# Kernel optimization log

Hardware: AMD Instinct MI355X
Metric: run time of the kernel (lower is better)

## Reference

```python
import jax, jax.numpy as jnp
import numpy as np

SCALING = 2.0
EPS = 1e-8


def setup_inputs() -> dict:
    key = jax.random.key(0)
    k_x, k_a, k_b = jax.random.split(key, 3)
    N, B, S, H, R = 8, 2, 2048, 4096, 64
    x = jax.random.normal(k_x, (B, S, H), dtype=jnp.float32)
    lora_A = jax.random.normal(k_a, (N, H, R), dtype=jnp.float32)
    # torch init is zeros for B, but use small random values so the norm-rescale path is exercised
    lora_B = jax.random.normal(k_b, (N, R, H), dtype=jnp.float32) * 0.02
    return {"x": x, "lora_A": lora_A, "lora_B": lora_B}


def reference(x, lora_A, lora_B):
    # x: [B,S,H]; lora_A: [N,H,R]; lora_B: [N,R,H]
    intermediate = jnp.einsum('bsh,nhr->nbsr', x, lora_A)          # [N,B,S,R]
    updates = jnp.einsum('nbsr,nrh->nbsh', intermediate, lora_B)   # [N,B,S,H]
    norms = jnp.linalg.norm(updates, axis=-1, keepdims=True) + EPS
    updates = updates / norms * SCALING
    return x[None] + updates                                       # [N,B,S,H]
```

## Files before the change

### kernel.cpp

```cpp
#include <hip/hip_runtime.h>
#include <hip/hip_bf16.h>

#define NL 8
#define HD 4096
#define RD 64
#define MD 4096
#define NGC 512

typedef __bf16 bf16x8 __attribute__((ext_vector_type(8)));
typedef float f32x4 __attribute__((ext_vector_type(4)));
typedef unsigned short ushort8 __attribute__((ext_vector_type(8)));
typedef float float4v __attribute__((ext_vector_type(4)));

__device__ __forceinline__ unsigned short f2bf(float f) {
    union { __hip_bfloat16 b; unsigned short u; } c;
    c.b = __float2bfloat16(f);
    return c.u;
}

__device__ __forceinline__ void gload_lds16(const void* g, void* l) {
    auto gp = (const __attribute__((address_space(1))) unsigned int*)(g);
    auto lp = (__attribute__((address_space(3))) unsigned int*)(l);
    __builtin_amdgcn_global_load_lds(gp, lp, 16, 0, 0);
}

__global__ __launch_bounds__(256) void k_prep(const float* __restrict__ A,
                                              const float* __restrict__ B,
                                              unsigned short* __restrict__ At,
                                              unsigned short* __restrict__ Bt) {
    __shared__ unsigned short T[64][65];
    int t = threadIdx.x;
    int bb = blockIdx.x;
    if (bb < 512) {
        int n = bb >> 6;
        int h0 = (bb & 63) << 6;
        const float* src = A + (size_t)n * HD * RD;
#pragma unroll
        for (int rep = 0; rep < 16; ++rep) {
            int flat = rep * 256 + t;
            int hh = flat >> 6, rr = flat & 63;
            T[hh][rr] = f2bf(src[(size_t)(h0 + hh) * RD + rr]);
        }
        __syncthreads();
#pragma unroll
        for (int rep = 0; rep < 16; ++rep) {
            int flat = rep * 256 + t;
            int rr = flat >> 6, hh = flat & 63;
            At[(size_t)(n * RD + rr) * HD + h0 + hh] = T[hh][rr];
        }
    } else {
        int b2 = bb - 512;
        int n = b2 >> 6;
        int h0 = (b2 & 63) << 6;
        const float* src = B + (size_t)n * RD * HD;
#pragma unroll
        for (int rep = 0; rep < 16; ++rep) {
            int flat = rep * 256 + t;
            int rr = flat >> 6, hh = flat & 63;
            T[rr][hh] = f2bf(src[(size_t)rr * HD + h0 + hh]);
        }
        __syncthreads();
        unsigned short* dst = Bt + (size_t)n * HD * RD;
#pragma unroll
        for (int rep = 0; rep < 16; ++rep) {
            int flat = rep * 256 + t;
            int hh = flat >> 6, rr = flat & 63;
            dst[(size_t)(h0 + hh) * RD + rr] = T[rr][hh];
        }
    }
}

__global__ __launch_bounds__(256) void k_gram(const float* __restrict__ B,
                                              float* __restrict__ Gp) {
    __shared__ float Bl[64][129];
    int t = threadIdx.x;
    int n = blockIdx.x >> 5;
    int c = blockIdx.x & 31;
    int k0 = c << 7;
    const float* src = B + (size_t)n * RD * HD + k0;
#pragma unroll
    for (int rep = 0; rep < 8; ++rep) {
        int flat = (rep * 256 + t) * 4;
        int rr = flat >> 7, hh = flat & 127;
        float4v v = *(const float4v*)(src + (size_t)rr * HD + hh);
        Bl[rr][hh] = v[0]; Bl[rr][hh + 1] = v[1];
        Bl[rr][hh + 2] = v[2]; Bl[rr][hh + 3] = v[3];
    }
    __syncthreads();
    int i0 = (t >> 4) << 2;
    int j0 = (t & 15) << 2;
    float acc[4][4];
#pragma unroll
    for (int a = 0; a < 4; ++a)
#pragma unroll
        for (int b = 0; b < 4; ++b) acc[a][b] = 0.f;
    for (int h = 0; h < 128; ++h) {
        float bi[4], bj[4];
#pragma unroll
        for (int a = 0; a < 4; ++a) { bi[a] = Bl[i0 + a][h]; bj[a] = Bl[j0 + a][h]; }
#pragma unroll
        for (int a = 0; a < 4; ++a)
#pragma unroll
            for (int b = 0; b < 4; ++b) acc[a][b] += bi[a] * bj[b];
    }
    float* g = Gp + (size_t)(n * 32 + c) * RD * RD;
#pragma unroll
    for (int a = 0; a < 4; ++a)
#pragma unroll
        for (int b = 0; b < 4; ++b)
            g[(i0 + a) * RD + j0 + b] = acc[a][b];
}

__global__ __launch_bounds__(256) void k_gram_reduce(const float* __restrict__ Gp,
                                                     float* __restrict__ G) {
    int idx = blockIdx.x * 256 + threadIdx.x;
    int n = idx >> 12;
    int rem = idx & 4095;
    const float* src = Gp + (size_t)n * 32 * 4096 + rem;
    float sum = 0.f;
#pragma unroll
    for (int c = 0; c < 32; ++c) sum += src[(size_t)c * 4096];
    G[idx] = sum;
}

__global__ __launch_bounds__(256) void k_gemm1(const float* __restrict__ x,
                                               const unsigned short* __restrict__ At,
                                               float* __restrict__ inter_p) {
    __shared__ unsigned short As[2][64 * 64];
    __shared__ unsigned short Bs[2][128 * 64];
    int t = threadIdx.x, lane = t & 63;
    int bid = blockIdx.x;
    int ks = bid & 1;
    int c0 = ((bid >> 1) & 3) * 128;
    int m0 = (bid >> 3) * 64;
    int kbase = ks * 2048;

    int sa_r0 = t >> 3, sa_sg = t & 7;
    int sa_sw = sa_sg ^ (sa_r0 & 7);
    const float* xrow0 = x + (size_t)(m0 + sa_r0) * HD + sa_sg * 8;
    const float* xrow1 = x + (size_t)(m0 + sa_r0 + 32) * HD + sa_sg * 8;

    int wv = t >> 6;
    int wm = (wv >> 1) * 32;
    int wc = (wv & 1) * 64;

    f32x4 acc[4][2];
#pragma unroll
    for (int cf = 0; cf < 4; ++cf)
#pragma unroll
        for (int mf = 0; mf < 2; ++mf) acc[cf][mf] = (f32x4){0.f, 0.f, 0.f, 0.f};

    {
#pragma unroll
        for (int q = 0; q < 4; ++q) {
            int flat = q * 256 + t;
            int cc = flat >> 3, sg = flat & 7;
            int sw = sg ^ (cc & 7);
            gload_lds16(At + (size_t)(c0 + cc) * HD + kbase + sw * 8,
                        (void*)&Bs[0][(q * 256 + (t & ~63)) * 8]);
        }
        float4v a0 = *(const float4v*)(xrow0 + kbase);
        float4v a1 = *(const float4v*)(xrow0 + kbase + 4);
        float4v b0 = *(const float4v*)(xrow1 + kbase);
        float4v b1 = *(const float4v*)(xrow1 + kbase + 4);
        ushort8 sva, svb;
#pragma unroll
        for (int j = 0; j < 4; ++j) {
            sva[j] = f2bf(a0[j]); sva[j + 4] = f2bf(a1[j]);
            svb[j] = f2bf(b0[j]); svb[j + 4] = f2bf(b1[j]);
        }
        *(ushort8*)&As[0][sa_r0 * 64 + sa_sw * 8] = sva;
        *(ushort8*)&As[0][(sa_r0 + 32) * 64 + sa_sw * 8] = svb;
    }
    __syncthreads();

    float4v pa0, pa1, pb0, pb1;
    for (int kt = 0; kt < 32; ++kt) {
        int cur = kt & 1;
        int knext = kbase + (kt + 1) * 64;
        if (kt < 31) {
#pragma unroll
            for (int q = 0; q < 4; ++q) {
                int flat = q * 256 + t;
                int cc = flat >> 3, sg = flat & 7;
                int sw = sg ^ (cc & 7);
                gload_lds16(At + (size_t)(c0 + cc) * HD + knext + sw * 8,
                            (void*)&Bs[cur ^ 1][(q * 256 + (t & ~63)) * 8]);
            }
            pa0 = *(const float4v*)(xrow0 + knext);
            pa1 = *(const float4v*)(xrow0 + knext + 4);
            pb0 = *(const float4v*)(xrow1 + knext);
            pb1 = *(const float4v*)(xrow1 + knext + 4);
        }
        const unsigned short* as = As[cur];
        const unsigned short* bs = Bs[cur];
#pragma unroll
        for (int kk = 0; kk < 2; ++kk) {
            int seg = kk * 4 + (lane >> 4);
            bf16x8 a_c[4], b_x[2];
#pragma unroll
            for (int cf = 0; cf < 4; ++cf) {
                int row = wc + cf * 16 + (lane & 15);
                a_c[cf] = *(const bf16x8*)&bs[row * 64 + (seg ^ (row & 7)) * 8];
            }
#pragma unroll
            for (int mf = 0; mf < 2; ++mf) {
                int col = wm + mf * 16 + (lane & 15);
                b_x[mf] = *(const bf16x8*)&as[col * 64 + (seg ^ (col & 7)) * 8];
            }
#pragma unroll
            for (int cf = 0; cf < 4; ++cf)
#pragma unroll
                for (int mf = 0; mf < 2; ++mf)
                    acc[cf][mf] = __builtin_amdgcn_mfma_f32_16x16x32_bf16(
                        a_c[cf], b_x[mf], acc[cf][mf], 0, 0, 0);
        }
        if (kt < 31) {
            ushort8 sva, svb;
#pragma unroll
            for (int j = 0; j < 4; ++j) {
                sva[j] = f2bf(pa0[j]); sva[j + 4] = f2bf(pa1[j]);
                svb[j] = f2bf(pb0[j]); svb[j + 4] = f2bf(pb1[j]);
            }
            *(ushort8*)&As[cur ^ 1][sa_r0 * 64 + sa_sw * 8] = sva;
            *(ushort8*)&As[cur ^ 1][(sa_r0 + 32) * 64 + sa_sw * 8] = svb;
        }
        __syncthreads();
    }
    float* dst = inter_p + (size_t)ks * MD * NGC;
#pragma unroll
    for (int mf = 0; mf < 2; ++mf) {
        int m = m0 + wm + mf * 16 + (lane & 15);
#pragma unroll
        for (int cf = 0; cf < 4; ++cf) {
            int c = c0 + wc + cf * 16 + (lane >> 4) * 4;
            *(float4v*)&dst[(size_t)m * NGC + c] = acc[cf][mf];
        }
    }
}

__global__ __launch_bounds__(256) void k_scale(const float* __restrict__ inter_p,
                                               const float* __restrict__ G,
                                               float* __restrict__ s,
                                               unsigned short* __restrict__ interbf) {
    __shared__ float Gs[64][65];
    __shared__ float Ib[4][8][64];
    int t = threadIdx.x, lane = t & 63, wv = t >> 6;
    int n = blockIdx.x >> 7;
    int m0 = (blockIdx.x & 127) << 5;
    const float* gsrc = G + n * 4096;
#pragma unroll
    for (int rep = 0; rep < 16; ++rep) {
        int flat = rep * 256 + t;
        Gs[flat >> 6][flat & 63] = gsrc[flat];
    }
#pragma unroll
    for (int r = 0; r < 8; ++r) {
        int m = m0 + wv * 8 + r;
        size_t off = (size_t)m * NGC + n * RD + lane;
        float Iv = inter_p[off] + inter_p[(size_t)MD * NGC + off];
        interbf[off] = f2bf(Iv);
        Ib[wv][r][lane] = Iv;
    }
    __syncthreads();
    float greg[64];
#pragma unroll
    for (int j = 0; j < 64; ++j) greg[j] = Gs[lane][j];
#pragma unroll
    for (int r = 0; r < 8; ++r) {
        const float* ib = Ib[wv][r];
        float t0 = 0.f, t1 = 0.f, t2 = 0.f, t3 = 0.f;
#pragma unroll
        for (int j = 0; j < 64; j += 4) {
            t0 += greg[j]     * ib[j];
            t1 += greg[j + 1] * ib[j + 1];
            t2 += greg[j + 2] * ib[j + 2];
            t3 += greg[j + 3] * ib[j + 3];
        }
        float pl = ((t0 + t1) + (t2 + t3)) * ib[lane];
#pragma unroll
        for (int o = 32; o; o >>= 1) pl += __shfl_xor(pl, o);
        if (lane == 0) {
            int m = m0 + wv * 8 + r;
            s[n * MD + m] = 2.0f / (sqrtf(fmaxf(pl, 0.f)) + 1e-8f);
        }
    }
}

__global__ __launch_bounds__(256, 2) void k_gemm2(const float* __restrict__ x,
                                                  const unsigned short* __restrict__ interbf,
                                                  const unsigned short* __restrict__ Bt,
                                                  const float* __restrict__ s,
                                                  float* __restrict__ out) {
    __shared__ unsigned short As[2][64 * 64];
    __shared__ unsigned short Bs[2][256 * 64];
    int t = threadIdx.x, lane = t & 63, wv = t >> 6;
    int b = blockIdx.x;
    int xcd = b & 7;
    int idx = b >> 3;
    int h0 = (xcd * 2 + (idx >> 6)) * 256;
    int m0 = (idx & 63) * 64;

    int wm = (wv >> 1) * 32;
    int wh = (wv & 1) * 128;

#pragma unroll
    for (int q = 0; q < 8; ++q) {
        int flat = q * 256 + t;
        int h = flat >> 3, sg = flat & 7;
        int sw = sg ^ (h & 7);
        gload_lds16(Bt + (size_t)(0 * HD + h0 + h) * RD + sw * 8,
                    (void*)&Bs[0][(q * 256 + (t & ~63)) * 8]);
    }
#pragma unroll
    for (int q = 0; q < 2; ++q) {
        int flat = q * 256 + t;
        int m = flat >> 3, sg = flat & 7;
        int sw = sg ^ (m & 7);
        gload_lds16(interbf + (size_t)(m0 + m) * NGC + 0 * RD + sw * 8,
                    (void*)&As[0][(q * 256 + (t & ~63)) * 8]);
    }
    float4v xv[2][8];
#pragma unroll
    for (int mf = 0; mf < 2; ++mf) {
        int m = m0 + wm + mf * 16 + (lane & 15);
#pragma unroll
        for (int hf = 0; hf < 8; ++hf) {
            int h = h0 + wh + hf * 16 + (lane >> 4) * 4;
            xv[mf][hf] = *(const float4v*)&x[(size_t)m * HD + h];
        }
    }
    asm volatile("s_waitcnt vmcnt(0)" ::: "memory");
    __syncthreads();

    for (int n = 0; n < NL; ++n) {
        int cur = n & 1;
        if (n < NL - 1) {
#pragma unroll
            for (int q = 0; q < 8; ++q) {
                int flat = q * 256 + t;
                int h = flat >> 3, sg = flat & 7;
                int sw = sg ^ (h & 7);
                gload_lds16(Bt + (size_t)((n + 1) * HD + h0 + h) * RD + sw * 8,
                            (void*)&Bs[cur ^ 1][(q * 256 + (t & ~63)) * 8]);
            }
#pragma unroll
            for (int q = 0; q < 2; ++q) {
                int flat = q * 256 + t;
                int m = flat >> 3, sg = flat & 7;
                int sw = sg ^ (m & 7);
                gload_lds16(interbf + (size_t)(m0 + m) * NGC + (n + 1) * RD + sw * 8,
                            (void*)&As[cur ^ 1][(q * 256 + (t & ~63)) * 8]);
            }
        }
        asm volatile("" ::: "memory");

        f32x4 acc[8][2];
#pragma unroll
        for (int hf = 0; hf < 8; ++hf)
#pragma unroll
            for (int mf = 0; mf < 2; ++mf) acc[hf][mf] = (f32x4){0.f, 0.f, 0.f, 0.f};

        const unsigned short* as = As[cur];
        const unsigned short* bs = Bs[cur];
#pragma unroll
        for (int kk = 0; kk < 2; ++kk) {
            int seg = kk * 4 + (lane >> 4);
            bf16x8 a_h[8], b_m[2];
#pragma unroll
            for (int hf = 0; hf < 8; ++hf) {
                int row = wh + hf * 16 + (lane & 15);
                a_h[hf] = *(const bf16x8*)&bs[row * 64 + (seg ^ (row & 7)) * 8];
            }
#pragma unroll
            for (int mf = 0; mf < 2; ++mf) {
                int col = wm + mf * 16 + (lane & 15);
                b_m[mf] = *(const bf16x8*)&as[col * 64 + (seg ^ (col & 7)) * 8];
            }
#pragma unroll
            for (int hf = 0; hf < 8; ++hf)
#pragma unroll
                for (int mf = 0; mf < 2; ++mf)
                    acc[hf][mf] = __builtin_amdgcn_mfma_f32_16x16x32_bf16(
                        a_h[hf], b_m[mf], acc[hf][mf], 0, 0, 0);
        }

        size_t obase = (size_t)n * MD * HD;
#pragma unroll
        for (int mf = 0; mf < 2; ++mf) {
            int m = m0 + wm + mf * 16 + (lane & 15);
            float sv = s[n * MD + m];
#pragma unroll
            for (int hf = 0; hf < 8; ++hf) {
                int h = h0 + wh + hf * 16 + (lane >> 4) * 4;
                float4v r;
#pragma unroll
                for (int j = 0; j < 4; ++j) r[j] = xv[mf][hf][j] + sv * acc[hf][mf][j];
                *(float4v*)&out[obase + (size_t)m * HD + h] = r;
            }
        }
        if (n < NL - 1) {
            asm volatile("s_waitcnt vmcnt(16)\n\ts_barrier" ::: "memory");
        }
    }
}

extern "C" void kernel_launch(void* const* d_in, const int* in_sizes, int n_in,
                              void* d_out, int out_size, void* d_ws, size_t ws_size,
                              hipStream_t stream) {
    const float* x = (const float*)d_in[0];
    const float* lA = (const float*)d_in[1];
    const float* lB = (const float*)d_in[2];
    float* out = (float*)d_out;
    char* ws = (char*)d_ws;
    unsigned short* At      = (unsigned short*)(ws);
    unsigned short* Bt      = (unsigned short*)(ws + 4194304);
    float*          inter_p = (float*)(ws + 8388608);
    float*          Gp      = (float*)(ws + 25165824);
    float*          G       = (float*)(ws + 29360128);
    float*          s       = (float*)(ws + 29491200);
    unsigned short* interbf = (unsigned short*)(ws + 29622272);

    k_prep<<<1024, 256, 0, stream>>>(lA, lB, At, Bt);
    k_gram<<<256, 256, 0, stream>>>(lB, Gp);
    k_gram_reduce<<<128, 256, 0, stream>>>(Gp, G);
    k_gemm1<<<512, 256, 0, stream>>>(x, At, inter_p);
    k_scale<<<1024, 256, 0, stream>>>(inter_p, G, s, interbf);
    k_gemm2<<<1024, 256, 0, stream>>>(x, interbf, Bt, s, out);
}
```

Baseline: 218.2 us.

## Merge prep/gram launches and widen gemm1 M-tile to 128 rows

Folds the weight transpose/convert and the partial Gram computation into one kernel, and runs the Gram reduction as extra blocks inside gemm1, cutting two kernel launches. gemm1's M tile doubles from 64 to 128 rows, with four 16-row fragments per wave, so each At tile loaded from global memory is reused across more rows. The price is more LDS and accumulator registers per block and half as many gemm1 blocks (256 instead of 512), which may leave the GPU under-occupied.

```diff
diff --git a/kernel.cpp b/kernel.cpp
--- a/kernel.cpp
+++ b/kernel.cpp
@@ -24,11 +24,13 @@
     __builtin_amdgcn_global_load_lds(gp, lp, 16, 0, 0);
 }
 
-__global__ __launch_bounds__(256) void k_prep(const float* __restrict__ A,
-                                              const float* __restrict__ B,
-                                              unsigned short* __restrict__ At,
-                                              unsigned short* __restrict__ Bt) {
-    __shared__ unsigned short T[64][65];
+__global__ __launch_bounds__(256) void k_setup(const float* __restrict__ A,
+                                               const float* __restrict__ B,
+                                               unsigned short* __restrict__ At,
+                                               unsigned short* __restrict__ Bt,
+                                               float* __restrict__ Gp) {
+    __shared__ float BUF[64 * 129];
+    unsigned short* T = (unsigned short*)BUF;
     int t = threadIdx.x;
     int bb = blockIdx.x;
     if (bb < 512) {
@@ -39,16 +41,16 @@
         for (int rep = 0; rep < 16; ++rep) {
             int flat = rep * 256 + t;
             int hh = flat >> 6, rr = flat & 63;
-            T[hh][rr] = f2bf(src[(size_t)(h0 + hh) * RD + rr]);
+            T[hh * 65 + rr] = f2bf(src[(size_t)(h0 + hh) * RD + rr]);
         }
         __syncthreads();
 #pragma unroll
         for (int rep = 0; rep < 16; ++rep) {
             int flat = rep * 256 + t;
             int rr = flat >> 6, hh = flat & 63;
-            At[(size_t)(n * RD + rr) * HD + h0 + hh] = T[hh][rr];
-        }
-    } else {
+            At[(size_t)(n * RD + rr) * HD + h0 + hh] = T[hh * 65 + rr];
+        }
+    } else if (bb < 1024) {
         int b2 = bb - 512;
         int n = b2 >> 6;
         int h0 = (b2 & 63) << 6;
@@ -57,7 +59,7 @@
         for (int rep = 0; rep < 16; ++rep) {
             int flat = rep * 256 + t;
             int rr = flat >> 6, hh = flat & 63;
-            T[rr][hh] = f2bf(src[(size_t)rr * HD + h0 + hh]);
+            T[rr * 65 + hh] = f2bf(src[(size_t)rr * HD + h0 + hh]);
         }
         __syncthreads();
         unsigned short* dst = Bt + (size_t)n * HD * RD;
@@ -65,90 +67,90 @@
         for (int rep = 0; rep < 16; ++rep) {
             int flat = rep * 256 + t;
             int hh = flat >> 6, rr = flat & 63;
-            dst[(size_t)(h0 + hh) * RD + rr] = T[rr][hh];
-        }
-    }
-}
-
-__global__ __launch_bounds__(256) void k_gram(const float* __restrict__ B,
-                                              float* __restrict__ Gp) {
-    __shared__ float Bl[64][129];
-    int t = threadIdx.x;
-    int n = blockIdx.x >> 5;
-    int c = blockIdx.x & 31;
-    int k0 = c << 7;
-    const float* src = B + (size_t)n * RD * HD + k0;
-#pragma unroll
-    for (int rep = 0; rep < 8; ++rep) {
-        int flat = (rep * 256 + t) * 4;
-        int rr = flat >> 7, hh = flat & 127;
-        float4v v = *(const float4v*)(src + (size_t)rr * HD + hh);
-        Bl[rr][hh] = v[0]; Bl[rr][hh + 1] = v[1];
-        Bl[rr][hh + 2] = v[2]; Bl[rr][hh + 3] = v[3];
-    }
-    __syncthreads();
-    int i0 = (t >> 4) << 2;
-    int j0 = (t & 15) << 2;
-    float acc[4][4];
-#pragma unroll
-    for (int a = 0; a < 4; ++a)
-#pragma unroll
-        for (int b = 0; b < 4; ++b) acc[a][b] = 0.f;
-    for (int h = 0; h < 128; ++h) {
-        float bi[4], bj[4];
-#pragma unroll
-        for (int a = 0; a < 4; ++a) { bi[a] = Bl[i0 + a][h]; bj[a] = Bl[j0 + a][h]; }
+            dst[(size_t)(h0 + hh) * RD + rr] = T[rr * 65 + hh];
+        }
+    } else {
+        int g = bb - 1024;
+        int n = g >> 5;
+        int c = g & 31;
+        int k0 = c << 7;
+        float* Bl = BUF;
+        const float* src = B + (size_t)n * RD * HD + k0;
+#pragma unroll
+        for (int rep = 0; rep < 8; ++rep) {
+            int flat = (rep * 256 + t) * 4;
+            int rr = flat >> 7, hh = flat & 127;
+            float4v v = *(const float4v*)(src + (size_t)rr * HD + hh);
+            Bl[rr * 129 + hh] = v[0]; Bl[rr * 129 + hh + 1] = v[1];
+            Bl[rr * 129 + hh + 2] = v[2]; Bl[rr * 129 + hh + 3] = v[3];
+        }
+        __syncthreads();
+        int i0 = (t >> 4) << 2;
+        int j0 = (t & 15) << 2;
+        float acc[4][4];
 #pragma unroll
         for (int a = 0; a < 4; ++a)
 #pragma unroll
-            for (int b = 0; b < 4; ++b) acc[a][b] += bi[a] * bj[b];
-    }
-    float* g = Gp + (size_t)(n * 32 + c) * RD * RD;
-#pragma unroll
-    for (int a = 0; a < 4; ++a)
-#pragma unroll
-        for (int b = 0; b < 4; ++b)
-            g[(i0 + a) * RD + j0 + b] = acc[a][b];
-}
-
-__global__ __launch_bounds__(256) void k_gram_reduce(const float* __restrict__ Gp,
-                                                     float* __restrict__ G) {
-    int idx = blockIdx.x * 256 + threadIdx.x;
-    int n = idx >> 12;
-    int rem = idx & 4095;
-    const float* src = Gp + (size_t)n * 32 * 4096 + rem;
-    float sum = 0.f;
-#pragma unroll
-    for (int c = 0; c < 32; ++c) sum += src[(size_t)c * 4096];
-    G[idx] = sum;
+            for (int b = 0; b < 4; ++b) acc[a][b] = 0.f;
+        for (int h = 0; h < 128; ++h) {
+            float bi[4], bj[4];
+#pragma unroll
+            for (int a = 0; a < 4; ++a) { bi[a] = Bl[(i0 + a) * 129 + h]; bj[a] = Bl[(j0 + a) * 129 + h]; }
+#pragma unroll
+            for (int a = 0; a < 4; ++a)
+#pragma unroll
+                for (int b = 0; b < 4; ++b) acc[a][b] += bi[a] * bj[b];
+        }
+        float* gdst = Gp + (size_t)(n * 32 + c) * RD * RD;
+#pragma unroll
+        for (int a = 0; a < 4; ++a)
+#pragma unroll
+            for (int b = 0; b < 4; ++b)
+                gdst[(i0 + a) * RD + j0 + b] = acc[a][b];
+    }
 }
 
 __global__ __launch_bounds__(256) void k_gemm1(const float* __restrict__ x,
                                                const unsigned short* __restrict__ At,
-                                               float* __restrict__ inter_p) {
-    __shared__ unsigned short As[2][64 * 64];
+                                               float* __restrict__ inter_p,
+                                               const float* __restrict__ Gp,
+                                               float* __restrict__ G) {
+    __shared__ unsigned short As[2][128 * 64];
     __shared__ unsigned short Bs[2][128 * 64];
     int t = threadIdx.x, lane = t & 63;
     int bid = blockIdx.x;
+    if (bid >= 256) {
+        int idx = (bid - 256) * 256 + t;
+        int n = idx >> 12;
+        int rem = idx & 4095;
+        const float* src = Gp + (size_t)n * 32 * 4096 + rem;
+        float sum = 0.f;
+#pragma unroll
+        for (int c = 0; c < 32; ++c) sum += src[(size_t)c * 4096];
+        G[idx] = sum;
+        return;
+    }
     int ks = bid & 1;
     int c0 = ((bid >> 1) & 3) * 128;
-    int m0 = (bid >> 3) * 64;
+    int m0 = (bid >> 3) * 128;
     int kbase = ks * 2048;
 
-    int sa_r0 = t >> 3, sa_sg = t & 7;
-    int sa_sw = sa_sg ^ (sa_r0 & 7);
-    const float* xrow0 = x + (size_t)(m0 + sa_r0) * HD + sa_sg * 8;
-    const float* xrow1 = x + (size_t)(m0 + sa_r0 + 32) * HD + sa_sg * 8;
+    int sa_r = t >> 3, sa_sg = t & 7;
+    int sa_sw = sa_sg ^ (sa_r & 7);
+    const float* xrow[4];
+#pragma unroll
+    for (int j = 0; j < 4; ++j)
+        xrow[j] = x + (size_t)(m0 + sa_r + 32 * j) * HD + sa_sg * 8;
 
     int wv = t >> 6;
-    int wm = (wv >> 1) * 32;
+    int wm = (wv >> 1) * 64;
     int wc = (wv & 1) * 64;
 
-    f32x4 acc[4][2];
+    f32x4 acc[4][4];
 #pragma unroll
     for (int cf = 0; cf < 4; ++cf)
 #pragma unroll
-        for (int mf = 0; mf < 2; ++mf) acc[cf][mf] = (f32x4){0.f, 0.f, 0.f, 0.f};
+        for (int mf = 0; mf < 4; ++mf) acc[cf][mf] = (f32x4){0.f, 0.f, 0.f, 0.f};
 
     {
 #pragma unroll
@@ -159,22 +161,19 @@
             gload_lds16(At + (size_t)(c0 + cc) * HD + kbase + sw * 8,
                         (void*)&Bs[0][(q * 256 + (t & ~63)) * 8]);
         }
-        float4v a0 = *(const float4v*)(xrow0 + kbase);
-        float4v a1 = *(const float4v*)(xrow0 + kbase + 4);
-        float4v b0 = *(const float4v*)(xrow1 + kbase);
-        float4v b1 = *(const float4v*)(xrow1 + kbase + 4);
-        ushort8 sva, svb;
 #pragma unroll
         for (int j = 0; j < 4; ++j) {
-            sva[j] = f2bf(a0[j]); sva[j + 4] = f2bf(a1[j]);
-            svb[j] = f2bf(b0[j]); svb[j + 4] = f2bf(b1[j]);
-        }
-        *(ushort8*)&As[0][sa_r0 * 64 + sa_sw * 8] = sva;
-        *(ushort8*)&As[0][(sa_r0 + 32) * 64 + sa_sw * 8] = svb;
+            float4v v0 = *(const float4v*)(xrow[j] + kbase);
+            float4v v1 = *(const float4v*)(xrow[j] + kbase + 4);
+            ushort8 sv;
+#pragma unroll
+            for (int q = 0; q < 4; ++q) { sv[q] = f2bf(v0[q]); sv[q + 4] = f2bf(v1[q]); }
+            *(ushort8*)&As[0][(sa_r + 32 * j) * 64 + sa_sw * 8] = sv;
+        }
     }
     __syncthreads();
 
-    float4v pa0, pa1, pb0, pb1;
+    float4v pa[4][2];
     for (int kt = 0; kt < 32; ++kt) {
         int cur = kt & 1;
         int knext = kbase + (kt + 1) * 64;
@@ -187,49 +186,49 @@
                 gload_lds16(At + (size_t)(c0 + cc) * HD + knext + sw * 8,
                             (void*)&Bs[cur ^ 1][(q * 256 + (t & ~63)) * 8]);
             }
-            pa0 = *(const float4v*)(xrow0 + knext);
-            pa1 = *(const float4v*)(xrow0 + knext + 4);
-            pb0 = *(const float4v*)(xrow1 + knext);
-            pb1 = *(const float4v*)(xrow1 + knext + 4);
+#pragma unroll
+            for (int j = 0; j < 4; ++j) {
+                pa[j][0] = *(const float4v*)(xrow[j] + knext);
+                pa[j][1] = *(const float4v*)(xrow[j] + knext + 4);
+            }
         }
         const unsigned short* as = As[cur];
         const unsigned short* bs = Bs[cur];
 #pragma unroll
         for (int kk = 0; kk < 2; ++kk) {
             int seg = kk * 4 + (lane >> 4);
-            bf16x8 a_c[4], b_x[2];
+            bf16x8 a_c[4], b_x[4];
 #pragma unroll
             for (int cf = 0; cf < 4; ++cf) {
                 int row = wc + cf * 16 + (lane & 15);
                 a_c[cf] = *(const bf16x8*)&bs[row * 64 + (seg ^ (row & 7)) * 8];
             }
 #pragma unroll
-            for (int mf = 0; mf < 2; ++mf) {
+            for (int mf = 0; mf < 4; ++mf) {
                 int col = wm + mf * 16 + (lane & 15);
                 b_x[mf] = *(const bf16x8*)&as[col * 64 + (seg ^ (col & 7)) * 8];
             }
 #pragma unroll
             for (int cf = 0; cf < 4; ++cf)
 #pragma unroll
-                for (int mf = 0; mf < 2; ++mf)
+                for (int mf = 0; mf < 4; ++mf)
                     acc[cf][mf] = __builtin_amdgcn_mfma_f32_16x16x32_bf16(
                         a_c[cf], b_x[mf], acc[cf][mf], 0, 0, 0);
         }
         if (kt < 31) {
-            ushort8 sva, svb;
 #pragma unroll
             for (int j = 0; j < 4; ++j) {
-                sva[j] = f2bf(pa0[j]); sva[j + 4] = f2bf(pa1[j]);
-                svb[j] = f2bf(pb0[j]); svb[j + 4] = f2bf(pb1[j]);
-            }
-            *(ushort8*)&As[cur ^ 1][sa_r0 * 64 + sa_sw * 8] = sva;
-            *(ushort8*)&As[cur ^ 1][(sa_r0 + 32) * 64 + sa_sw * 8] = svb;
+                ushort8 sv;
+#pragma unroll
+                for (int q = 0; q < 4; ++q) { sv[q] = f2bf(pa[j][0][q]); sv[q + 4] = f2bf(pa[j][1][q]); }
+                *(ushort8*)&As[cur ^ 1][(sa_r + 32 * j) * 64 + sa_sw * 8] = sv;
+            }
         }
         __syncthreads();
     }
     float* dst = inter_p + (size_t)ks * MD * NGC;
 #pragma unroll
-    for (int mf = 0; mf < 2; ++mf) {
+    for (int mf = 0; mf < 4; ++mf) {
         int m = m0 + wm + mf * 16 + (lane & 15);
 #pragma unroll
         for (int cf = 0; cf < 4; ++cf) {
@@ -421,10 +420,8 @@
     float*          s       = (float*)(ws + 29491200);
     unsigned short* interbf = (unsigned short*)(ws + 29622272);
 
-    k_prep<<<1024, 256, 0, stream>>>(lA, lB, At, Bt);
-    k_gram<<<256, 256, 0, stream>>>(lB, Gp);
-    k_gram_reduce<<<128, 256, 0, stream>>>(Gp, G);
-    k_gemm1<<<512, 256, 0, stream>>>(x, At, inter_p);
+    k_setup<<<1280, 256, 0, stream>>>(lA, lB, At, Bt, Gp);
+    k_gemm1<<<384, 256, 0, stream>>>(x, At, inter_p, Gp, G);
     k_scale<<<1024, 256, 0, stream>>>(inter_p, G, s, interbf);
     k_gemm2<<<1024, 256, 0, stream>>>(x, interbf, Bt, s, out);
 }
```

Result: slower. 239.2 us (+9.6%).
